# Kernel optimization log

Measured on AMD Instinct MI355X. Metric: run time of the kernel, lower is better.

## Reference

```python
import jax, jax.numpy as jnp
import numpy as np

B, N, D, E, H = 128, 64, 128, 32, 256

def setup_inputs() -> dict:
    key = jax.random.key(0)
    ks = jax.random.split(key, 6)
    nodes = jax.random.normal(ks[0], (B, N, D), dtype=jnp.float32)
    edges = jax.random.normal(ks[1], (B, N * N, E), dtype=jnp.float32)
    W1 = jax.random.normal(ks[2], (2 * D + E, H), dtype=jnp.float32) * (1.0 / np.sqrt(2 * D + E))
    b1 = jnp.zeros((H,), dtype=jnp.float32)
    W2 = jax.random.normal(ks[3], (H, H), dtype=jnp.float32) * (1.0 / np.sqrt(H))
    b2 = jnp.zeros((H,), dtype=jnp.float32)
    W3 = jax.random.normal(ks[4], (H, 1), dtype=jnp.float32) * (1.0 / np.sqrt(H))
    b3 = jnp.zeros((1,), dtype=jnp.float32)
    return {"nodes": nodes, "edges": edges, "W1": W1, "b1": b1, "W2": W2, "b2": b2, "W3": W3, "b3": b3}

def reference(nodes, edges, W1, b1, W2, b2, W3, b3):
    b, n, d = nodes.shape
    # state_i[p] = nodes[p // n] (each node repeated n times consecutively)
    state_i = jnp.broadcast_to(nodes[:, :, None, :], (b, n, n, d)).reshape(b, n * n, d)
    # state_j[p] = nodes[p % n] (whole node list tiled n times)
    state_j = jnp.broadcast_to(nodes[:, None, :, :], (b, n, n, d)).reshape(b, n * n, d)
    concat = jnp.concatenate([state_i, edges, state_j], axis=-1)  # [b, n*n, 2d+e]
    a1 = jax.nn.relu(jnp.einsum('bpf,fh->bph', concat, W1) + b1)
    a2 = jax.nn.relu(jnp.einsum('bph,hk->bpk', a1, W2) + b2)
    return jnp.einsum('bph,ho->bpo', a2, W3) + b3  # [b, n*n, 1]
```

## Files before the change

kernel.cpp:

```cpp
#include <hip/hip_runtime.h>
#include <hip/hip_bf16.h>

typedef __bf16 bf16_t;
typedef __bf16 bf16x8 __attribute__((ext_vector_type(8)));
typedef float  f32x4  __attribute__((ext_vector_type(4)));

static __device__ __forceinline__ f32x4 mfma16(bf16x8 a, bf16x8 b, f32x4 c) {
    return __builtin_amdgcn_mfma_f32_16x16x32_bf16(a, b, c, 0, 0, 0);
}

__global__ void prep_pack(const float* __restrict__ W1, const float* __restrict__ W2,
                          bf16_t* __restrict__ W1ef, bf16_t* __restrict__ W2f) {
    int t = blockIdx.x * blockDim.x + threadIdx.x;
    int l = t & 63, g = l >> 4, c = l & 15;
    if (t < 1024) {
        int ht = t >> 6;
        int hcol = 32 * (ht >> 1) + 8 * (c >> 2) + 4 * (ht & 1) + (c & 3);
        #pragma unroll
        for (int j = 0; j < 8; ++j)
            W1ef[t * 8 + j] = (bf16_t)W1[(128 + 8 * g + j) * 256 + hcol];
    } else if (t < 1024 + 8192) {
        int t2 = t - 1024;
        int ks = t2 >> 10;
        int ct = (t2 >> 6) & 15;
        #pragma unroll
        for (int j = 0; j < 8; ++j) {
            int krow = 32 * ks + 8 * g + 4 * (j >> 2) + (j & 3);
            W2f[t2 * 8 + j] = (bf16_t)W2[krow * 256 + ct * 16 + c];
        }
    }
}

__global__ __launch_bounds__(256) void prep_pij(const float* __restrict__ nodes,
                                                const float* __restrict__ W1,
                                                const float* __restrict__ b1,
                                                float* __restrict__ Pi,
                                                bf16_t* __restrict__ Pjb) {
    int b = blockIdx.x >> 2;
    int q = blockIdx.x & 3;
    int h = threadIdx.x;
    const float* nb = nodes + (b * 64 + q * 16) * 128;
    float ai[16], aj[16];
    float bias = b1[h];
    #pragma unroll
    for (int ii = 0; ii < 16; ++ii) { ai[ii] = bias; aj[ii] = 0.f; }
    for (int d = 0; d < 128; ++d) {
        float wi = W1[d * 256 + h];
        float wj = W1[(160 + d) * 256 + h];
        #pragma unroll
        for (int ii = 0; ii < 16; ++ii) {
            float s = nb[ii * 128 + d];
            ai[ii] = fmaf(s, wi, ai[ii]);
            aj[ii] = fmaf(s, wj, aj[ii]);
        }
    }
    #pragma unroll
    for (int ii = 0; ii < 16; ++ii) {
        Pi[(b * 64 + q * 16 + ii) * 256 + h] = ai[ii];
        Pjb[(b * 64 + q * 16 + ii) * 256 + h] = (bf16_t)aj[ii];
    }
}

__global__ __launch_bounds__(512, 2) void mlp_main(
    const float* __restrict__ edges,
    const float* __restrict__ Pi, const bf16_t* __restrict__ Pjb,
    const bf16_t* __restrict__ W1ef, const bf16_t* __restrict__ W2f,
    const float* __restrict__ b2, const float* __restrict__ W3,
    const float* __restrict__ b3, float* __restrict__ out) {

    __shared__ bf16_t a1f[2][16384];
    __shared__ bf16_t elds[2][2048];
    __shared__ float part[2][8][64];

    const int p = blockIdx.x;
    const int xb = (p & 7) * 64 + (p >> 3);
    const int tid = threadIdx.x;
    const int w = tid >> 6, l = tid & 63, g = l >> 4, c = l & 15;
    const int b = xb >> 2;
    const f32x4 z4 = {0.f, 0.f, 0.f, 0.f};

    bf16x8 wf[2];
    #pragma unroll
    for (int z = 0; z < 2; ++z)
        wf[z] = *(const bf16x8*)&W1ef[((2 * w + z) * 64 + l) * 8];

    bf16x8 pjb[4];
    #pragma unroll
    for (int pt = 0; pt < 4; ++pt)
        pjb[pt] = *(const bf16x8*)&Pjb[((long)(b * 64 + 16 * pt + c)) * 256
                                       + 32 * w + 8 * g];

    const float bias3 = b3[0];

    const int spt = tid >> 6, sg = (tid >> 4) & 3, sc = tid & 15;
    const long erowbase = (long)xb * 1024 + 16 * spt + sc;

    f32x4 es0, es1;
    if (tid < 256) {
        const float* ep = edges + erowbase * 32 + 8 * sg;
        es0 = *(const f32x4*)ep; es1 = *(const f32x4*)(ep + 4);
    }
    const float* PiB = Pi + ((long)xb * 16) * 256 + 32 * w + 8 * g;
    f32x4 pva0 = *(const f32x4*)PiB;
    f32x4 pva1 = *(const f32x4*)(PiB + 4);

    if (tid < 256) {
        bf16x8 ev;
        #pragma unroll
        for (int j = 0; j < 4; ++j) { ev[j] = (bf16_t)es0[j]; ev[4 + j] = (bf16_t)es1[j]; }
        *(bf16x8*)&elds[0][tid * 8] = ev;
    }
    __syncthreads();

    f32x4 pvb0, pvb1;

    for (int t = 0; t < 16; ++t) {
        const int cur = t & 1;

        if (t < 15) {
            if (tid < 256) {
                const float* ep = edges + (erowbase + 64 * (t + 1)) * 32 + 8 * sg;
                es0 = *(const f32x4*)ep; es1 = *(const f32x4*)(ep + 4);
            }
            const float* pp = PiB + (t + 1) * 256;
            pvb0 = *(const f32x4*)pp; pvb1 = *(const f32x4*)(pp + 4);
        }

        {
            bf16x8 ebf[4];
            #pragma unroll
            for (int pt = 0; pt < 4; ++pt)
                ebf[pt] = *(const bf16x8*)&elds[cur][(pt * 64 + l) * 8];
            #pragma unroll
            for (int pt = 0; pt < 4; ++pt) {
                bf16x8 o;
                #pragma unroll
                for (int z = 0; z < 2; ++z) {
                    f32x4 a = mfma16(wf[z], ebf[pt], z4);
                    f32x4 pv = z ? pva1 : pva0;
                    #pragma unroll
                    for (int r = 0; r < 4; ++r) {
                        float v = a[r] + pv[r] + (float)pjb[pt][4 * z + r];
                        v = v > 0.f ? v : 0.f;
                        o[4 * z + r] = (bf16_t)v;
                    }
                }
                *(bf16x8*)&a1f[cur][((pt * 8 + w) * 64 + l) * 8] = o;
            }
        }

        if (t < 15 && tid < 256) {
            bf16x8 ev;
            #pragma unroll
            for (int j = 0; j < 4; ++j) { ev[j] = (bf16_t)es0[j]; ev[4 + j] = (bf16_t)es1[j]; }
            *(bf16x8*)&elds[cur ^ 1][tid * 8] = ev;
        }
        __syncthreads();

        if (t > 0 && tid < 64) {
            float s = bias3;
            #pragma unroll
            for (int ww = 0; ww < 8; ++ww) s += part[cur ^ 1][ww][tid];
            out[(long)xb * 1024 + (t - 1) * 64 + tid] = s;
        }

        {
            f32x4 acc2[4][2];
            #pragma unroll
            for (int pt = 0; pt < 4; ++pt) { acc2[pt][0] = z4; acc2[pt][1] = z4; }
            #pragma unroll
            for (int ks = 0; ks < 8; ++ks) {
                bf16x8 af[4];
                #pragma unroll
                for (int pt = 0; pt < 4; ++pt)
                    af[pt] = *(const bf16x8*)&a1f[cur][((pt * 8 + ks) * 64 + l) * 8];
                #pragma unroll
                for (int cc = 0; cc < 2; ++cc) {
                    bf16x8 w2 = *(const bf16x8*)&W2f[((ks * 16 + 2 * w + cc) * 64 + l) * 8];
                    #pragma unroll
                    for (int pt = 0; pt < 4; ++pt)
                        acc2[pt][cc] = mfma16(w2, af[pt], acc2[pt][cc]);
                }
            }
            f32x4 b2q[2], w3q[2];
            #pragma unroll
            for (int cc = 0; cc < 2; ++cc) {
                b2q[cc] = *(const f32x4*)&b2[32 * w + 16 * cc + 4 * g];
                w3q[cc] = *(const f32x4*)&W3[32 * w + 16 * cc + 4 * g];
            }
            #pragma unroll
            for (int pt = 0; pt < 4; ++pt) {
                float s = 0.f;
                #pragma unroll
                for (int cc = 0; cc < 2; ++cc)
                    #pragma unroll
                    for (int r = 0; r < 4; ++r) {
                        float v = acc2[pt][cc][r] + b2q[cc][r];
                        v = v > 0.f ? v : 0.f;
                        s = fmaf(v, w3q[cc][r], s);
                    }
                s += __shfl_xor(s, 16);
                s += __shfl_xor(s, 32);
                if (g == 0) part[cur][w][pt * 16 + c] = s;
            }
        }
        pva0 = pvb0; pva1 = pvb1;
    }

    __syncthreads();
    if (tid < 64) {
        float s = bias3;
        #pragma unroll
        for (int ww = 0; ww < 8; ++ww) s += part[1][ww][tid];
        out[(long)xb * 1024 + 15 * 64 + tid] = s;
    }
}

extern "C" void kernel_launch(void* const* d_in, const int* in_sizes, int n_in,
                              void* d_out, int out_size, void* d_ws, size_t ws_size,
                              hipStream_t stream) {
    const float* nodes = (const float*)d_in[0];
    const float* edges = (const float*)d_in[1];
    const float* W1    = (const float*)d_in[2];
    const float* b1    = (const float*)d_in[3];
    const float* W2    = (const float*)d_in[4];
    const float* b2    = (const float*)d_in[5];
    const float* W3    = (const float*)d_in[6];
    const float* b3    = (const float*)d_in[7];
    float* out = (float*)d_out;

    char* ws = (char*)d_ws;
    float*  Pi   = (float*)ws;
    bf16_t* Pjb  = (bf16_t*)(ws + (size_t)8 * 1024 * 1024);
    bf16_t* W2f  = (bf16_t*)(ws + (size_t)12 * 1024 * 1024);
    bf16_t* W1ef = (bf16_t*)(ws + (size_t)12 * 1024 * 1024 + 131072);

    prep_pack<<<dim3(36), dim3(256), 0, stream>>>(W1, W2, W1ef, W2f);
    prep_pij<<<dim3(512), dim3(256), 0, stream>>>(nodes, W1, b1, Pi, Pjb);
    mlp_main<<<dim3(512), dim3(512), 0, stream>>>(edges, Pi, Pjb, W1ef, W2f, b2, W3, b3, out);
}
```

Before: 111.0 us.

## Warp-specialize mlp_main into layer-1 producer and layer-2 consumer waves

Splits the 8 waves of each block into two groups. Four waves build the layer-1 activations and stage the edge tiles. The other four run the layer-2 MFMA GEMM and the W3 reduction on the previous tile, one step behind, so the two stages overlap across a 17-step loop. Each group now does twice the per-wave work (4 weight fragments / 4 output column tiles), which raises register pressure and halves the parallelism inside each stage. The partial-sum buffers shrink to four entries.

```diff
diff --git a/kernel.cpp b/kernel.cpp
--- a/kernel.cpp
+++ b/kernel.cpp
@@ -70,149 +70,150 @@
 
     __shared__ bf16_t a1f[2][16384];
     __shared__ bf16_t elds[2][2048];
-    __shared__ float part[2][8][64];
+    __shared__ float part[2][4][64];
 
     const int p = blockIdx.x;
     const int xb = (p & 7) * 64 + (p >> 3);
     const int tid = threadIdx.x;
     const int w = tid >> 6, l = tid & 63, g = l >> 4, c = l & 15;
+    const int rw = w & 3;
     const int b = xb >> 2;
     const f32x4 z4 = {0.f, 0.f, 0.f, 0.f};
-
-    bf16x8 wf[2];
-    #pragma unroll
-    for (int z = 0; z < 2; ++z)
-        wf[z] = *(const bf16x8*)&W1ef[((2 * w + z) * 64 + l) * 8];
-
-    bf16x8 pjb[4];
-    #pragma unroll
-    for (int pt = 0; pt < 4; ++pt)
-        pjb[pt] = *(const bf16x8*)&Pjb[((long)(b * 64 + 16 * pt + c)) * 256
-                                       + 32 * w + 8 * g];
-
     const float bias3 = b3[0];
-
-    const int spt = tid >> 6, sg = (tid >> 4) & 3, sc = tid & 15;
-    const long erowbase = (long)xb * 1024 + 16 * spt + sc;
-
-    f32x4 es0, es1;
-    if (tid < 256) {
-        const float* ep = edges + erowbase * 32 + 8 * sg;
-        es0 = *(const f32x4*)ep; es1 = *(const f32x4*)(ep + 4);
-    }
-    const float* PiB = Pi + ((long)xb * 16) * 256 + 32 * w + 8 * g;
-    f32x4 pva0 = *(const f32x4*)PiB;
-    f32x4 pva1 = *(const f32x4*)(PiB + 4);
-
-    if (tid < 256) {
-        bf16x8 ev;
-        #pragma unroll
-        for (int j = 0; j < 4; ++j) { ev[j] = (bf16_t)es0[j]; ev[4 + j] = (bf16_t)es1[j]; }
-        *(bf16x8*)&elds[0][tid * 8] = ev;
-    }
-    __syncthreads();
-
-    f32x4 pvb0, pvb1;
-
-    for (int t = 0; t < 16; ++t) {
-        const int cur = t & 1;
-
-        if (t < 15) {
-            if (tid < 256) {
-                const float* ep = edges + (erowbase + 64 * (t + 1)) * 32 + 8 * sg;
-                es0 = *(const f32x4*)ep; es1 = *(const f32x4*)(ep + 4);
-            }
-            const float* pp = PiB + (t + 1) * 256;
-            pvb0 = *(const f32x4*)pp; pvb1 = *(const f32x4*)(pp + 4);
-        }
-
+    const long outbase = (long)xb * 1024;
+
+    if (w < 4) {
+        bf16x8 wf[4];
+        #pragma unroll
+        for (int q = 0; q < 4; ++q)
+            wf[q] = *(const bf16x8*)&W1ef[((4 * rw + q) * 64 + l) * 8];
+
+        bf16x8 pjb[4][2];
+        #pragma unroll
+        for (int pt = 0; pt < 4; ++pt)
+            #pragma unroll
+            for (int o = 0; o < 2; ++o)
+                pjb[pt][o] = *(const bf16x8*)&Pjb[((long)(b * 64 + 16 * pt + c)) * 256
+                                                  + 32 * (2 * rw + o) + 8 * g];
+
+        const int sg = (tid >> 4) & 3, sc = tid & 15;
+        const long erowbase = (long)xb * 1024 + 16 * rw + sc;
+
+        f32x4 es0, es1;
         {
-            bf16x8 ebf[4];
-            #pragma unroll
-            for (int pt = 0; pt < 4; ++pt)
-                ebf[pt] = *(const bf16x8*)&elds[cur][(pt * 64 + l) * 8];
-            #pragma unroll
-            for (int pt = 0; pt < 4; ++pt) {
-                bf16x8 o;
-                #pragma unroll
-                for (int z = 0; z < 2; ++z) {
-                    f32x4 a = mfma16(wf[z], ebf[pt], z4);
-                    f32x4 pv = z ? pva1 : pva0;
-                    #pragma unroll
-                    for (int r = 0; r < 4; ++r) {
-                        float v = a[r] + pv[r] + (float)pjb[pt][4 * z + r];
-                        v = v > 0.f ? v : 0.f;
-                        o[4 * z + r] = (bf16_t)v;
-                    }
-                }
-                *(bf16x8*)&a1f[cur][((pt * 8 + w) * 64 + l) * 8] = o;
-            }
-        }
-
-        if (t < 15 && tid < 256) {
+            const float* ep = edges + erowbase * 32 + 8 * sg;
+            es0 = *(const f32x4*)ep; es1 = *(const f32x4*)(ep + 4);
             bf16x8 ev;
             #pragma unroll
             for (int j = 0; j < 4; ++j) { ev[j] = (bf16_t)es0[j]; ev[4 + j] = (bf16_t)es1[j]; }
-            *(bf16x8*)&elds[cur ^ 1][tid * 8] = ev;
+            *(bf16x8*)&elds[0][tid * 8] = ev;
         }
         __syncthreads();
 
-        if (t > 0 && tid < 64) {
+        for (int t = 0; t < 17; ++t) {
+            const int cur = t & 1;
+            if (t < 16) {
+                if (t < 15) {
+                    const float* ep = edges + (erowbase + 64 * (t + 1)) * 32 + 8 * sg;
+                    es0 = *(const f32x4*)ep; es1 = *(const f32x4*)(ep + 4);
+                }
+                const float* PiB = Pi + ((long)xb * 16 + t) * 256;
+                f32x4 piv[2][2];
+                #pragma unroll
+                for (int o = 0; o < 2; ++o) {
+                    const float* pp = PiB + 32 * (2 * rw + o) + 8 * g;
+                    piv[o][0] = *(const f32x4*)pp;
+                    piv[o][1] = *(const f32x4*)(pp + 4);
+                }
+                bf16x8 ebf[4];
+                #pragma unroll
+                for (int pt = 0; pt < 4; ++pt)
+                    ebf[pt] = *(const bf16x8*)&elds[cur][(pt * 64 + l) * 8];
+                #pragma unroll
+                for (int pt = 0; pt < 4; ++pt) {
+                    #pragma unroll
+                    for (int o = 0; o < 2; ++o) {
+                        bf16x8 oct;
+                        #pragma unroll
+                        for (int z = 0; z < 2; ++z) {
+                            f32x4 a = mfma16(wf[2 * o + z], ebf[pt], z4);
+                            #pragma unroll
+                            for (int r = 0; r < 4; ++r) {
+                                float v = a[r] + piv[o][z][r] + (float)pjb[pt][o][4 * z + r];
+                                v = v > 0.f ? v : 0.f;
+                                oct[4 * z + r] = (bf16_t)v;
+                            }
+                        }
+                        *(bf16x8*)&a1f[cur][((pt * 8 + 2 * rw + o) * 64 + l) * 8] = oct;
+                    }
+                }
+                if (t < 15) {
+                    bf16x8 ev;
+                    #pragma unroll
+                    for (int j = 0; j < 4; ++j) { ev[j] = (bf16_t)es0[j]; ev[4 + j] = (bf16_t)es1[j]; }
+                    *(bf16x8*)&elds[cur ^ 1][tid * 8] = ev;
+                }
+            }
+            if (t >= 2 && tid < 64) {
+                float s = bias3;
+                #pragma unroll
+                for (int cw = 0; cw < 4; ++cw) s += part[cur][cw][tid];
+                out[outbase + (t - 2) * 64 + tid] = s;
+            }
+            __syncthreads();
+        }
+        if (tid < 64) {
             float s = bias3;
             #pragma unroll
-            for (int ww = 0; ww < 8; ++ww) s += part[cur ^ 1][ww][tid];
-            out[(long)xb * 1024 + (t - 1) * 64 + tid] = s;
-        }
-
-        {
-            f32x4 acc2[4][2];
-            #pragma unroll
-            for (int pt = 0; pt < 4; ++pt) { acc2[pt][0] = z4; acc2[pt][1] = z4; }
-            #pragma unroll
-            for (int ks = 0; ks < 8; ++ks) {
-                bf16x8 af[4];
+            for (int cw = 0; cw < 4; ++cw) s += part[1][cw][tid];
+            out[outbase + 15 * 64 + tid] = s;
+        }
+    } else {
+        __syncthreads();
+
+        for (int t = 0; t < 17; ++t) {
+            if (t >= 1) {
+                const int buf = (t - 1) & 1;
+                f32x4 acc2[4][4];
                 #pragma unroll
                 for (int pt = 0; pt < 4; ++pt)
-                    af[pt] = *(const bf16x8*)&a1f[cur][((pt * 8 + ks) * 64 + l) * 8];
-                #pragma unroll
-                for (int cc = 0; cc < 2; ++cc) {
-                    bf16x8 w2 = *(const bf16x8*)&W2f[((ks * 16 + 2 * w + cc) * 64 + l) * 8];
+                    #pragma unroll
+                    for (int cc = 0; cc < 4; ++cc) acc2[pt][cc] = z4;
+                #pragma unroll
+                for (int ks = 0; ks < 8; ++ks) {
+                    bf16x8 af[4];
                     #pragma unroll
                     for (int pt = 0; pt < 4; ++pt)
-                        acc2[pt][cc] = mfma16(w2, af[pt], acc2[pt][cc]);
+                        af[pt] = *(const bf16x8*)&a1f[buf][((pt * 8 + ks) * 64 + l) * 8];
+                    #pragma unroll
+                    for (int cc = 0; cc < 4; ++cc) {
+                        bf16x8 w2 = *(const bf16x8*)&W2f[((ks * 16 + 4 * rw + cc) * 64 + l) * 8];
+                        #pragma unroll
+                        for (int pt = 0; pt < 4; ++pt)
+                            acc2[pt][cc] = mfma16(w2, af[pt], acc2[pt][cc]);
+                    }
+                }
+                #pragma unroll
+                for (int pt = 0; pt < 4; ++pt) {
+                    float s = 0.f;
+                    #pragma unroll
+                    for (int cc = 0; cc < 4; ++cc) {
+                        f32x4 b2q = *(const f32x4*)&b2[64 * rw + 16 * cc + 4 * g];
+                        f32x4 w3q = *(const f32x4*)&W3[64 * rw + 16 * cc + 4 * g];
+                        #pragma unroll
+                        for (int r = 0; r < 4; ++r) {
+                            float v = acc2[pt][cc][r] + b2q[r];
+                            v = v > 0.f ? v : 0.f;
+                            s = fmaf(v, w3q[r], s);
+                        }
+                    }
+                    s += __shfl_xor(s, 16);
+                    s += __shfl_xor(s, 32);
+                    if (g == 0) part[buf][rw][pt * 16 + c] = s;
                 }
             }
-            f32x4 b2q[2], w3q[2];
-            #pragma unroll
-            for (int cc = 0; cc < 2; ++cc) {
-                b2q[cc] = *(const f32x4*)&b2[32 * w + 16 * cc + 4 * g];
-                w3q[cc] = *(const f32x4*)&W3[32 * w + 16 * cc + 4 * g];
-            }
-            #pragma unroll
-            for (int pt = 0; pt < 4; ++pt) {
-                float s = 0.f;
-                #pragma unroll
-                for (int cc = 0; cc < 2; ++cc)
-                    #pragma unroll
-                    for (int r = 0; r < 4; ++r) {
-                        float v = acc2[pt][cc][r] + b2q[cc][r];
-                        v = v > 0.f ? v : 0.f;
-                        s = fmaf(v, w3q[cc][r], s);
-                    }
-                s += __shfl_xor(s, 16);
-                s += __shfl_xor(s, 32);
-                if (g == 0) part[cur][w][pt * 16 + c] = s;
-            }
-        }
-        pva0 = pvb0; pva1 = pvb1;
-    }
-
-    __syncthreads();
-    if (tid < 64) {
-        float s = bias3;
-        #pragma unroll
-        for (int ww = 0; ww < 8; ++ww) s += part[1][ww][tid];
-        out[(long)xb * 1024 + 15 * 64 + tid] = s;
+            __syncthreads();
+        }
     }
 }
 
```

Result: slower. 122.4 us (+10.2%).
